# Performance work log

Measured on AMD Instinct MI355X. Metric: run time of the kernel, lower is better.

Reference implementation:

```python
import jax, jax.numpy as jnp
import numpy as np

B, T, D = 4, 2048, 2048
NH, NKV, HD = 8, 4, 256
SOFT_CAP = 50.0
ROPE_BASE = 10000
K_MASK = -2.3819763e38


def apply_rope(x, positions, base_frequency):
    # x: [b, t, n, h], positions: [b, t]
    head_dim = x.shape[-1]
    fraction = 2.0 * jnp.arange(head_dim // 2, dtype=jnp.float32) / head_dim
    timescale = base_frequency ** fraction  # [h/2]
    sinusoid = positions[..., None].astype(jnp.float32) / timescale  # [b, t, h/2]
    sinusoid = sinusoid[..., None, :]  # [b, t, 1, h/2]
    sin, cos = jnp.sin(sinusoid), jnp.cos(sinusoid)
    x1, x2 = jnp.split(x, 2, axis=-1)
    out = jnp.concatenate([x1 * cos - x2 * sin, x2 * cos + x1 * sin], axis=-1)
    return out.astype(x.dtype)


def setup_inputs() -> dict:
    key = jax.random.key(0)
    k1, k2, k3 = jax.random.split(key, 3)
    x = jax.random.normal(k1, (B, T, D), dtype=jnp.float32)
    positions = jnp.broadcast_to(jnp.arange(T, dtype=jnp.int32), (B, T))
    # causal mask, broadcast over kv-head axis
    causal = jnp.tril(jnp.ones((T, T), dtype=bool))
    attn_mask = jnp.broadcast_to(causal[None, None], (B, 1, T, T))
    w_qkv = jax.random.normal(k2, (D, (NH + 2 * NKV) * HD), dtype=jnp.float32) * (D ** -0.5)
    w_out = jax.random.normal(k3, (NH * HD, D), dtype=jnp.float32) * ((NH * HD) ** -0.5)
    return {"x": x, "positions": positions, "attn_mask": attn_mask,
            "w_qkv": w_qkv, "w_out": w_out}


def reference(x, positions, attn_mask, w_qkv, w_out):
    b, t, _ = x.shape
    g = NH // NKV  # queries per kv head
    qkv = x @ w_qkv  # [b, t, (NH+2*NKV)*HD]
    q, k, v = jnp.split(qkv, [NH * HD, (NH + NKV) * HD], axis=-1)
    q = q.reshape(b, t, NH, HD)
    k = k.reshape(b, t, NKV, HD)
    v = v.reshape(b, t, NKV, HD)
    q = apply_rope(q, positions, ROPE_BASE)
    k = apply_rope(k, positions, ROPE_BASE)
    q_grouped = q.reshape(b, t, NKV, g, HD)
    logits = jnp.einsum('btkgh,bskh->bkgts', q_grouped, k,
                        preferred_element_type=jnp.float32)
    # soft-cap BEFORE scaling (faithful to source order)
    logits = jnp.tanh(logits / SOFT_CAP) * SOFT_CAP
    logits = logits / jnp.sqrt(jnp.float32(HD))
    final_mask = attn_mask[:, :, None, :, :]  # [b, 1, 1, t, s]
    masked = jnp.where(final_mask, logits, K_MASK)
    probs = jax.nn.softmax(masked, axis=-1).astype(x.dtype)
    encoded = jnp.einsum('bkgts,bskh->btkgh', probs, v)
    encoded = encoded.reshape(b, t, NH * HD)
    return encoded @ w_out
```

## Files before the change

### kernel.cpp

```cpp
#include <hip/hip_runtime.h>
#include <hip/hip_bf16.h>

typedef unsigned short u16;
typedef unsigned int   u32;
typedef __bf16 bf16x8 __attribute__((ext_vector_type(8)));
typedef float  f32x4  __attribute__((ext_vector_type(4)));

static constexpr int B_ = 4, T_ = 2048, D_ = 2048, NH_ = 8, NKV_ = 4, HD_ = 256;
static constexpr int QKVC = (NH_ + 2 * NKV_) * HD_;
static constexpr int ENC_C = NH_ * HD_;

__device__ __forceinline__ u16 f2b(float f) {
  u32 x = __float_as_uint(f);
  return (u16)((x + 0x7fffu + ((x >> 16) & 1u)) >> 16);
}
__device__ __forceinline__ float b2f(u16 u) { return __uint_as_float(((u32)u) << 16); }

__device__ __forceinline__ void gload_lds16(const void* g, void* l) {
  __builtin_amdgcn_global_load_lds((const __attribute__((address_space(1))) void*)g,
                                   (__attribute__((address_space(3))) void*)l, 16, 0, 0);
}

__global__ void cvt_f32_bf16(const float* __restrict__ in, u16* __restrict__ out, int n) {
  for (size_t i = ((size_t)blockIdx.x * 256 + threadIdx.x) * 8; i < (size_t)n;
       i += (size_t)gridDim.x * 256 * 8) {
    float4 a = *(const float4*)(in + i);
    float4 b = *(const float4*)(in + i + 4);
    u16 t[8] = {f2b(a.x), f2b(a.y), f2b(a.z), f2b(a.w), f2b(b.x), f2b(b.y), f2b(b.z), f2b(b.w)};
    *(uint4*)(out + i) = *(const uint4*)t;
  }
}

__global__ void transpose_cvt(const float* __restrict__ src, u16* __restrict__ dst, int R, int C) {
  __shared__ u16 tl[64][72];
  const int c0 = blockIdx.x << 6, r0 = blockIdx.y << 6;
  const int tid = threadIdx.x;
  const int lr = tid >> 2, lc = (tid & 3) << 4;
  const float* p = src + (size_t)(r0 + lr) * C + c0 + lc;
#pragma unroll
  for (int j = 0; j < 16; j += 4) {
    float4 v = *(const float4*)(p + j);
    tl[lr][lc + j + 0] = f2b(v.x);
    tl[lr][lc + j + 1] = f2b(v.y);
    tl[lr][lc + j + 2] = f2b(v.z);
    tl[lr][lc + j + 3] = f2b(v.w);
  }
  __syncthreads();
  u16 tmp[16];
#pragma unroll
  for (int j = 0; j < 16; j++) tmp[j] = tl[lc + j][lr];
  u16* q = dst + (size_t)(c0 + lr) * R + r0 + lc;
  *(uint4*)q = *(const uint4*)tmp;
  *(uint4*)(q + 8) = *(const uint4*)(tmp + 8);
}

__global__ void vt_build(const u16* __restrict__ qkv, u16* __restrict__ vt) {
  __shared__ u16 tl[64][72];
  const int t0 = blockIdx.x << 6, d0 = blockIdx.y << 6, z = blockIdx.z;
  const int tid = threadIdx.x;
  const int lr = tid >> 2, lc = (tid & 3) << 4;
  const u16* p = qkv + (size_t)((z >> 2) * T_ + t0 + lr) * QKVC + (NH_ + NKV_) * HD_ +
                 (z & 3) * HD_ + d0 + lc;
#pragma unroll
  for (int j = 0; j < 16; j++) tl[lr][lc + j] = p[j];
  __syncthreads();
  u16 tmp[16];
#pragma unroll
  for (int j = 0; j < 16; j++) tmp[j] = tl[lc + j][lr];
  u16* q = vt + ((size_t)z * HD_ + d0 + lr) * T_ + t0 + lc;
  *(uint4*)q = *(const uint4*)tmp;
  *(uint4*)(q + 8) = *(const uint4*)(tmp + 8);
}

__global__ void rope_inplace(u16* __restrict__ qkv, const int* __restrict__ positions) {
  const int row = blockIdx.x;
  const float pos = (float)positions[row];
  u16* base = qkv + (size_t)row * QKVC;
  for (int it = threadIdx.x; it < 12 * 128; it += 256) {
    const int head = it >> 7, i = it & 127;
    const int cb = head * HD_;
    const float inv = exp2f(-(float)i * 0.10381025296522975f);
    const float ang = pos * inv;
    float s, c;
    __sincosf(ang, &s, &c);
    const float x1 = b2f(base[cb + i]), x2 = b2f(base[cb + 128 + i]);
    base[cb + i]       = f2b(x1 * c - x2 * s);
    base[cb + 128 + i] = f2b(x2 * c + x1 * s);
  }
}

template <bool OUT_F32>
__global__ __launch_bounds__(256, 2) void gemm_bt(const u16* __restrict__ A,
                                                  const u16* __restrict__ Bt,
                                                  void* __restrict__ Cp, int M, int N, int K) {
  __shared__ __align__(16) u16 Al[2][128 * 32];
  __shared__ __align__(16) u16 Bl[2][128 * 32];
  const int tid = threadIdx.x;
  const int w = tid >> 6, l = tid & 63;
  const int lr = l & 15, khi = l >> 4;
  const size_t bm = (size_t)blockIdx.y << 7, bn = (size_t)blockIdx.x << 7;
  const int mrow = (w >> 1) << 6, ncol = (w & 1) << 6;
  f32x4 acc[4][4] = {};
  const int nt = K >> 5;

  auto stage = [&](int buf, int k0) {
#pragma unroll
    for (int j = 0; j < 2; j++) {
      const int p = j * 256 + tid;
      const int row = p >> 2, slot = p & 3;
      const int dk = slot ^ ((row >> 1) & 3);
      gload_lds16(A + (bm + row) * K + k0 + dk * 8, &Al[buf][(j * 256 + (w << 6)) * 8]);
      gload_lds16(Bt + (bn + row) * K + k0 + dk * 8, &Bl[buf][(j * 256 + (w << 6)) * 8]);
    }
  };

  stage(0, 0);
  for (int t = 0; t < nt; ++t) {
    const int cur = t & 1;
    __syncthreads();
    if (t + 1 < nt) stage(cur ^ 1, (t + 1) << 5);
    bf16x8 aF[4], bF[4];
#pragma unroll
    for (int mf = 0; mf < 4; mf++) {
      const int r = mrow + (mf << 4) + lr;
      const int slot = khi ^ ((r >> 1) & 3);
      aF[mf] = *(const bf16x8*)&Al[cur][r * 32 + slot * 8];
    }
#pragma unroll
    for (int nf = 0; nf < 4; nf++) {
      const int c = ncol + (nf << 4) + lr;
      const int slot = khi ^ ((c >> 1) & 3);
      bF[nf] = *(const bf16x8*)&Bl[cur][c * 32 + slot * 8];
    }
#pragma unroll
    for (int mf = 0; mf < 4; mf++)
#pragma unroll
      for (int nf = 0; nf < 4; nf++)
        acc[mf][nf] = __builtin_amdgcn_mfma_f32_16x16x32_bf16(aF[mf], bF[nf], acc[mf][nf], 0, 0, 0);
  }
#pragma unroll
  for (int mf = 0; mf < 4; mf++) {
#pragma unroll
    for (int j = 0; j < 4; j++) {
      const size_t row = bm + mrow + (mf << 4) + (khi << 2) + j;
#pragma unroll
      for (int nf = 0; nf < 4; nf++) {
        const size_t col = bn + ncol + (nf << 4) + lr;
        if constexpr (OUT_F32)
          ((float*)Cp)[row * N + col] = acc[mf][nf][j];
        else
          ((u16*)Cp)[row * N + col] = f2b(acc[mf][nf][j]);
      }
    }
  }
}

__global__ __launch_bounds__(256, 2) void attn_kernel(const u16* __restrict__ qkv,
                                                      const u16* __restrict__ VT,
                                                      u16* __restrict__ enc) {
  __shared__ __align__(16) u16 Kl[64 * 256];
  __shared__ __align__(16) u16 Vl[256 * 64];
  __shared__ __align__(16) u16 Pl[4][16 * 72];
  const int tid = threadIdx.x, w = tid >> 6, l = tid & 63;
  const int lr = l & 15, khi = l >> 4;
  const int qt = blockIdx.x, bh = blockIdx.y;
  const int b = bh >> 3, h = bh & 7, kv = h >> 1;
  const int q0 = qt << 6;
  const int tq = q0 + (w << 4) + lr;

  const u16* qrow = qkv + (size_t)(b * T_ + tq) * QKVC + h * HD_;
  bf16x8 qf[8];
#pragma unroll
  for (int ks = 0; ks < 8; ks++) qf[ks] = *(const bf16x8*)(qrow + ks * 32 + khi * 8);

  f32x4 opv[16] = {};
  float m_run[4], l_run[4];
#pragma unroll
  for (int j = 0; j < 4; j++) { m_run[j] = -3.0e38f; l_run[j] = 0.f; }

  const u16* Kbase = qkv + (size_t)b * T_ * QKVC + NH_ * HD_ + kv * HD_;
  const u16* Vbase = VT + (size_t)(b * NKV_ + kv) * HD_ * T_;
  const int nst = qt + 1;

  for (int st = 0; st < nst; ++st) {
    const int s0 = st << 6;
#pragma unroll
    for (int i = 0; i < 8; i++) {
      const int p = i * 256 + tid;
      const int row = p >> 5, slot = p & 31;
      const int dk = slot ^ (row & 7);
      gload_lds16(Kbase + (size_t)(s0 + row) * QKVC + dk * 8, &Kl[(i * 256 + (w << 6)) * 8]);
    }
#pragma unroll
    for (int i = 0; i < 8; i++) {
      const int p = i * 256 + tid;
      const int row = p >> 3, slot = p & 7;
      const int dk = slot ^ (row & 7);
      gload_lds16(Vbase + (size_t)row * T_ + s0 + dk * 8, &Vl[(i * 256 + (w << 6)) * 8]);
    }
    __syncthreads();

    f32x4 aqk[4] = {};
#pragma unroll
    for (int ks = 0; ks < 8; ks++) {
#pragma unroll
      for (int nf = 0; nf < 4; nf++) {
        const int c = (nf << 4) + lr;
        const int slot = (ks * 4 + khi) ^ (c & 7);
        bf16x8 bk = *(const bf16x8*)&Kl[c * 256 + slot * 8];
        aqk[nf] = __builtin_amdgcn_mfma_f32_16x16x32_bf16(qf[ks], bk, aqk[nf], 0, 0, 0);
      }
    }

#pragma unroll
    for (int j = 0; j < 4; j++) {
      const int t = q0 + (w << 4) + (khi << 2) + j;
      float lg[4];
      float mx = -3.0e38f;
#pragma unroll
      for (int nf = 0; nf < 4; nf++) {
        const int s = s0 + (nf << 4) + lr;
        float r = aqk[nf][j] * 0.02f;
        r = fminf(fmaxf(r, -15.f), 15.f);
        const float e2 = __expf(r + r);
        float v = (e2 - 1.f) / (e2 + 1.f) * 3.125f;
        v = (s <= t) ? v : -3.0e38f;
        lg[nf] = v;
        mx = fmaxf(mx, v);
      }
#pragma unroll
      for (int o = 1; o < 16; o <<= 1) mx = fmaxf(mx, __shfl_xor(mx, o));
      const float mnew = fmaxf(m_run[j], mx);
      const float scale = __expf(m_run[j] - mnew);
      float rs = 0.f;
#pragma unroll
      for (int nf = 0; nf < 4; nf++) {
        const float p = __expf(lg[nf] - mnew);
        rs += p;
        Pl[w][((khi << 2) + j) * 72 + (nf << 4) + lr] = f2b(p);
      }
#pragma unroll
      for (int o = 1; o < 16; o <<= 1) rs += __shfl_xor(rs, o);
      l_run[j] = l_run[j] * scale + rs;
      m_run[j] = mnew;
#pragma unroll
      for (int nf = 0; nf < 16; nf++) opv[nf][j] *= scale;
    }
    __syncthreads();

#pragma unroll
    for (int ks = 0; ks < 2; ks++) {
      bf16x8 ap = *(const bf16x8*)&Pl[w][lr * 72 + ks * 32 + khi * 8];
#pragma unroll
      for (int nf = 0; nf < 16; nf++) {
        const int hd = (nf << 4) + lr;
        const int slot = ((ks << 2) + khi) ^ (hd & 7);
        bf16x8 bv = *(const bf16x8*)&Vl[hd * 64 + slot * 8];
        opv[nf] = __builtin_amdgcn_mfma_f32_16x16x32_bf16(ap, bv, opv[nf], 0, 0, 0);
      }
    }
    __syncthreads();
  }

  float rl[4];
#pragma unroll
  for (int j = 0; j < 4; j++) rl[j] = 1.0f / l_run[j];
#pragma unroll
  for (int nf = 0; nf < 16; nf++) {
#pragma unroll
    for (int j = 0; j < 4; j++) {
      const int t = q0 + (w << 4) + (khi << 2) + j;
      enc[(size_t)(b * T_ + t) * ENC_C + h * HD_ + (nf << 4) + lr] = f2b(opv[nf][j] * rl[j]);
    }
  }
}

extern "C" void kernel_launch(void* const* d_in, const int* in_sizes, int n_in,
                              void* d_out, int out_size, void* d_ws, size_t ws_size,
                              hipStream_t stream) {
  const float* x = (const float*)d_in[0];
  const int* positions = (const int*)d_in[1];
  const float* w_qkv = (const float*)d_in[3];
  const float* w_out = (const float*)d_in[4];
  float* out = (float*)d_out;

  char* ws = (char*)d_ws;
  u16* X16 = (u16*)(ws + 0);
  u16* WQT = (u16*)(ws + 33554432);
  u16* WOT = (u16*)(ws + 50331648);
  u16* QKV = (u16*)(ws + 58720256);
  u16* VT  = (u16*)(ws + 125829120);
  u16* ENC = X16;

  cvt_f32_bf16<<<2048, 256, 0, stream>>>(x, X16, B_ * T_ * D_);
  {
    dim3 g(QKVC / 64, D_ / 64);
    transpose_cvt<<<g, 256, 0, stream>>>(w_qkv, WQT, D_, QKVC);
  }
  {
    dim3 g(D_ / 64, ENC_C / 64);
    transpose_cvt<<<g, 256, 0, stream>>>(w_out, WOT, ENC_C, D_);
  }
  {
    dim3 g(QKVC / 128, (B_ * T_) / 128);
    gemm_bt<false><<<g, 256, 0, stream>>>(X16, WQT, QKV, B_ * T_, QKVC, D_);
  }
  rope_inplace<<<B_ * T_, 256, 0, stream>>>(QKV, positions);
  {
    dim3 g(T_ / 64, HD_ / 64, B_ * NKV_);
    vt_build<<<g, 256, 0, stream>>>(QKV, VT);
  }
  {
    dim3 g(T_ / 64, B_ * NH_);
    attn_kernel<<<g, 256, 0, stream>>>(QKV, VT, ENC);
  }
  {
    dim3 g(D_ / 128, (B_ * T_) / 128);
    gemm_bt<true><<<g, 256, 0, stream>>>(ENC, WOT, out, B_ * T_, D_, ENC_C);
  }
}
```

Before: 755.1 us.

## Rewrite attention without LDS or online max, using register-resident P

The attention kernel drops LDS staging and the online-softmax max tracking. Because the soft cap bounds the logits, it exponentiates against a fixed offset, and the running max, rescaling and per-tile shuffles go away. QK^T is computed with K as the A operand so each lane's probabilities already sit in the PV MFMA operand layout; they are packed to bf16 by truncation with perm instead of a round trip through shared memory. K and V fragments are read straight from global memory, which removes the barriers but means each wave refetches K/V, relying on cache. The launch also remaps blocks per XCD, runs the longest causal tiles first, and allows 3 blocks per CU.

Measured after the change: 1.034 ms. 37.0% more time.

```diff
diff --git a/kernel.cpp b/kernel.cpp
--- a/kernel.cpp
+++ b/kernel.cpp
@@ -155,124 +155,92 @@
   }
 }
 
-__global__ __launch_bounds__(256, 2) void attn_kernel(const u16* __restrict__ qkv,
+__global__ __launch_bounds__(256, 3) void attn_kernel(const u16* __restrict__ qkv,
                                                       const u16* __restrict__ VT,
                                                       u16* __restrict__ enc) {
-  __shared__ __align__(16) u16 Kl[64 * 256];
-  __shared__ __align__(16) u16 Vl[256 * 64];
-  __shared__ __align__(16) u16 Pl[4][16 * 72];
   const int tid = threadIdx.x, w = tid >> 6, l = tid & 63;
   const int lr = l & 15, khi = l >> 4;
-  const int qt = blockIdx.x, bh = blockIdx.y;
-  const int b = bh >> 3, h = bh & 7, kv = h >> 1;
-  const int q0 = qt << 6;
-  const int tq = q0 + (w << 4) + lr;
-
-  const u16* qrow = qkv + (size_t)(b * T_ + tq) * QKVC + h * HD_;
+  const int id = blockIdx.x;
+  const int xcd = id & 7, slot = id >> 3;
+  const int g = xcd + ((slot >> 6) << 3), sub = slot & 63;
+  const int b = g >> 2, kv = g & 3;
+  const int h = (kv << 1) + (sub & 1);
+  const int qt = 31 - (sub >> 1);
+  const int qw = (qt << 6) + (w << 4);
+  const int tq = qw + lr;
+
+  const u16* qrow = qkv + (size_t)(b * T_ + tq) * QKVC + h * HD_ + khi * 8;
   bf16x8 qf[8];
 #pragma unroll
-  for (int ks = 0; ks < 8; ks++) qf[ks] = *(const bf16x8*)(qrow + ks * 32 + khi * 8);
+  for (int kk = 0; kk < 8; kk++) qf[kk] = *(const bf16x8*)(qrow + kk * 32);
+
+  const u16* Kbase = qkv + (size_t)b * T_ * QKVC + NH_ * HD_ + kv * HD_ + khi * 8;
+  const u16* Vbase = VT + (size_t)(b * NKV_ + kv) * HD_ * T_;
 
   f32x4 opv[16] = {};
-  float m_run[4], l_run[4];
-#pragma unroll
-  for (int j = 0; j < 4; j++) { m_run[j] = -3.0e38f; l_run[j] = 0.f; }
-
-  const u16* Kbase = qkv + (size_t)b * T_ * QKVC + NH_ * HD_ + kv * HD_;
-  const u16* Vbase = VT + (size_t)(b * NKV_ + kv) * HD_ * T_;
-  const int nst = qt + 1;
-
-  for (int st = 0; st < nst; ++st) {
+  float lsum = 0.f;
+  const int srow_lo = ((lr >> 2) << 3) + (lr & 3);
+
+  for (int st = 0; st <= qt; ++st) {
     const int s0 = st << 6;
-#pragma unroll
-    for (int i = 0; i < 8; i++) {
-      const int p = i * 256 + tid;
-      const int row = p >> 5, slot = p & 31;
-      const int dk = slot ^ (row & 7);
-      gload_lds16(Kbase + (size_t)(s0 + row) * QKVC + dk * 8, &Kl[(i * 256 + (w << 6)) * 8]);
-    }
-#pragma unroll
-    for (int i = 0; i < 8; i++) {
-      const int p = i * 256 + tid;
-      const int row = p >> 3, slot = p & 7;
-      const int dk = slot ^ (row & 7);
-      gload_lds16(Vbase + (size_t)row * T_ + s0 + dk * 8, &Vl[(i * 256 + (w << 6)) * 8]);
-    }
-    __syncthreads();
-
-    f32x4 aqk[4] = {};
-#pragma unroll
-    for (int ks = 0; ks < 8; ks++) {
-#pragma unroll
-      for (int nf = 0; nf < 4; nf++) {
-        const int c = (nf << 4) + lr;
-        const int slot = (ks * 4 + khi) ^ (c & 7);
-        bf16x8 bk = *(const bf16x8*)&Kl[c * 256 + slot * 8];
-        aqk[nf] = __builtin_amdgcn_mfma_f32_16x16x32_bf16(qf[ks], bk, aqk[nf], 0, 0, 0);
-      }
-    }
-
-#pragma unroll
-    for (int j = 0; j < 4; j++) {
-      const int t = q0 + (w << 4) + (khi << 2) + j;
-      float lg[4];
-      float mx = -3.0e38f;
-#pragma unroll
-      for (int nf = 0; nf < 4; nf++) {
-        const int s = s0 + (nf << 4) + lr;
-        float r = aqk[nf][j] * 0.02f;
-        r = fminf(fmaxf(r, -15.f), 15.f);
-        const float e2 = __expf(r + r);
-        float v = (e2 - 1.f) / (e2 + 1.f) * 3.125f;
-        v = (s <= t) ? v : -3.0e38f;
-        lg[nf] = v;
-        mx = fmaxf(mx, v);
-      }
-#pragma unroll
-      for (int o = 1; o < 16; o <<= 1) mx = fmaxf(mx, __shfl_xor(mx, o));
-      const float mnew = fmaxf(m_run[j], mx);
-      const float scale = __expf(m_run[j] - mnew);
-      float rs = 0.f;
-#pragma unroll
-      for (int nf = 0; nf < 4; nf++) {
-        const float p = __expf(lg[nf] - mnew);
-        rs += p;
-        Pl[w][((khi << 2) + j) * 72 + (nf << 4) + lr] = f2b(p);
-      }
-#pragma unroll
-      for (int o = 1; o < 16; o <<= 1) rs += __shfl_xor(rs, o);
-      l_run[j] = l_run[j] * scale + rs;
-      m_run[j] = mnew;
-#pragma unroll
-      for (int nf = 0; nf < 16; nf++) opv[nf][j] *= scale;
-    }
-    __syncthreads();
-
-#pragma unroll
-    for (int ks = 0; ks < 2; ks++) {
-      bf16x8 ap = *(const bf16x8*)&Pl[w][lr * 72 + ks * 32 + khi * 8];
-#pragma unroll
-      for (int nf = 0; nf < 16; nf++) {
-        const int hd = (nf << 4) + lr;
-        const int slot = ((ks << 2) + khi) ^ (hd & 7);
-        bf16x8 bv = *(const bf16x8*)&Vl[hd * 64 + slot * 8];
-        opv[nf] = __builtin_amdgcn_mfma_f32_16x16x32_bf16(ap, bv, opv[nf], 0, 0, 0);
-      }
-    }
-    __syncthreads();
-  }
-
-  float rl[4];
-#pragma unroll
-  for (int j = 0; j < 4; j++) rl[j] = 1.0f / l_run[j];
-#pragma unroll
-  for (int nf = 0; nf < 16; nf++) {
-#pragma unroll
-    for (int j = 0; j < 4; j++) {
-      const int t = q0 + (w << 4) + (khi << 2) + j;
-      enc[(size_t)(b * T_ + t) * ENC_C + h * HD_ + (nf << 4) + lr] = f2b(opv[nf][j] * rl[j]);
-    }
-  }
+    f32x4 pst[4];
+#pragma unroll
+    for (int sg = 0; sg < 4; ++sg) {
+      const int srow = s0 + ((sg >> 1) << 5) + ((sg & 1) << 2) + srow_lo;
+      const u16* kr = Kbase + (size_t)srow * QKVC;
+      f32x4 a = {};
+#pragma unroll
+      for (int kk = 0; kk < 8; kk++) {
+        bf16x8 kf = *(const bf16x8*)(kr + kk * 32);
+        a = __builtin_amdgcn_mfma_f32_16x16x32_bf16(kf, qf[kk], a, 0, 0, 0);
+      }
+      pst[sg] = a;
+    }
+    float part = 0.f;
+#pragma unroll
+    for (int sg = 0; sg < 4; ++sg) {
+#pragma unroll
+      for (int j = 0; j < 4; j++) {
+        const int s = s0 + ((sg >> 1) << 5) + (khi << 3) + ((sg & 1) << 2) + j;
+        const float e2 = __expf(pst[sg][j] * 0.04f);
+        float p = __expf(-6.25f * __builtin_amdgcn_rcpf(e2 + 1.f));
+        p = (s <= tq) ? p : 0.f;
+        pst[sg][j] = p;
+        part += p;
+      }
+    }
+    lsum += part;
+#pragma unroll
+    for (int ks = 0; ks < 2; ++ks) {
+      union { u32 u[4]; bf16x8 v; } ap;
+      ap.u[0] = __builtin_amdgcn_perm(__float_as_uint(pst[2 * ks][1]),
+                                      __float_as_uint(pst[2 * ks][0]), 0x07060302u);
+      ap.u[1] = __builtin_amdgcn_perm(__float_as_uint(pst[2 * ks][3]),
+                                      __float_as_uint(pst[2 * ks][2]), 0x07060302u);
+      ap.u[2] = __builtin_amdgcn_perm(__float_as_uint(pst[2 * ks + 1][1]),
+                                      __float_as_uint(pst[2 * ks + 1][0]), 0x07060302u);
+      ap.u[3] = __builtin_amdgcn_perm(__float_as_uint(pst[2 * ks + 1][3]),
+                                      __float_as_uint(pst[2 * ks + 1][2]), 0x07060302u);
+      const u16* vr = Vbase + (size_t)lr * T_ + s0 + (ks << 5) + (khi << 3);
+#pragma unroll
+      for (int nf = 0; nf < 16; ++nf) {
+        bf16x8 bv = *(const bf16x8*)(vr + (size_t)(nf << 4) * T_);
+        opv[nf] = __builtin_amdgcn_mfma_f32_16x16x32_bf16(ap.v, bv, opv[nf], 0, 0, 0);
+      }
+    }
+  }
+  lsum += __shfl_xor(lsum, 16);
+  lsum += __shfl_xor(lsum, 32);
+  const float rinv = 1.f / lsum;
+  float rj[4];
+#pragma unroll
+  for (int j = 0; j < 4; j++) rj[j] = __shfl(rinv, (khi << 2) + j);
+  u16* erow = enc + (size_t)(b * T_ + qw) * ENC_C + h * HD_ + lr;
+#pragma unroll
+  for (int nf = 0; nf < 16; ++nf)
+#pragma unroll
+    for (int j = 0; j < 4; j++)
+      erow[(size_t)((khi << 2) + j) * ENC_C + (nf << 4)] = f2b(opv[nf][j] * rj[j]);
 }
 
 extern "C" void kernel_launch(void* const* d_in, const int* in_sizes, int n_in,
@@ -310,10 +278,7 @@
     dim3 g(T_ / 64, HD_ / 64, B_ * NKV_);
     vt_build<<<g, 256, 0, stream>>>(QKV, VT);
   }
-  {
-    dim3 g(T_ / 64, B_ * NH_);
-    attn_kernel<<<g, 256, 0, stream>>>(QKV, VT, ENC);
-  }
+  attn_kernel<<<1024, 256, 0, stream>>>(QKV, VT, ENC);
   {
     dim3 g(D_ / 128, (B_ * T_) / 128);
     gemm_bt<true><<<g, 256, 0, stream>>>(ENC, WOT, out, B_ * T_, D_, ENC_C);
```
